# Kernel optimization log

Measured on AMD Instinct MI355X. Metric: run time of the kernel, lower is better.

## Reference

```python
import jax, jax.numpy as jnp
import numpy as np

N, E = 4096, 262144
IMG, EMB = 2048, 256        # img_feat_dim, embedding_dim*2
H, D = 4, 64                # heads, per-head out_channels (EMB//H for MHA too)
HID, C = 128, 2

def _sanitize(t):
    t = jnp.nan_to_num(t, nan=0.0, posinf=1000.0, neginf=-1000.0)
    return jnp.clip(t, -1000.0, 1000.0)

def _lrelu(t):
    return jax.nn.leaky_relu(t, 0.2)

def _instance_norm(y, eps=1e-5):
    # PyG InstanceNorm (affine=False), single graph: per-channel norm over nodes
    return (y - y.mean(0)) * jax.lax.rsqrt(y.var(0) + eps)

def _mha_causal(h, W_qkv, b_qkv, W_o, b_o):
    n = h.shape[0]
    qkv = h @ W_qkv.T + b_qkv
    q, k, v = jnp.split(qkv, 3, axis=-1)
    q = q.reshape(n, H, D); k = k.reshape(n, H, D); v = v.reshape(n, H, D)
    scores = jnp.einsum('qhd,khd->hqk', q, k) / np.float32(np.sqrt(D))
    mask = jnp.tril(jnp.ones((n, n), bool))
    scores = jnp.where(mask, scores, -jnp.inf)
    attn = jax.nn.softmax(scores, axis=-1)
    out = jnp.einsum('hqk,khd->qhd', attn, v).reshape(n, H * D)
    return out @ W_o.T + b_o

def _transformer_conv(xn, ei, Wq, bq, Wk, bk, Wv, bv, Ws, bs):
    # PyG TransformerConv: per-edge attention, softmax over incoming edges, +skip
    src, dst = ei[0], ei[1]
    n = xn.shape[0]
    q = (xn @ Wq.T + bq).reshape(n, H, D)
    k = (xn @ Wk.T + bk).reshape(n, H, D)
    v = (xn @ Wv.T + bv).reshape(n, H, D)
    logits = jnp.einsum('ehd,ehd->eh', q[dst], k[src]) / np.float32(np.sqrt(D))  # (E,H)
    amax = jax.ops.segment_max(logits, dst, num_segments=n)
    amax = jnp.where(jnp.isfinite(amax), amax, 0.0)
    ex = jnp.exp(logits - amax[dst])
    denom = jax.ops.segment_sum(ex, dst, num_segments=n)
    attn = ex / (denom[dst] + 1e-16)
    agg = jax.ops.segment_sum(attn[..., None] * v[src], dst, num_segments=n)
    return agg.reshape(n, H * D) + xn @ Ws.T + bs

def setup_inputs():
    key = jax.random.key(0)
    ks = jax.random.split(key, 20)
    w = lambda k, shape: jax.random.normal(k, shape, jnp.float32) * 0.02
    z = lambda d: jnp.zeros((d,), jnp.float32)
    return {
        'x': jax.random.normal(ks[0], (N, EMB), jnp.float32),
        'edge_index': jax.random.randint(ks[1], (2, E), 0, N),
        'img_feat': jax.random.normal(ks[2], (N, IMG), jnp.float32),
        'video_adj_list': jax.random.randint(ks[3], (2, E), 0, N),
        'W_img': w(ks[4], (EMB, IMG)), 'b_img': z(EMB),
        'W_qkv': w(ks[5], (3 * EMB, EMB)), 'b_qkv': z(3 * EMB),
        'W_o': w(ks[6], (EMB, EMB)), 'b_o': z(EMB),
        'Wq_o': w(ks[7], (H * D, EMB)), 'bq_o': z(H * D),
        'Wk_o': w(ks[8], (H * D, EMB)), 'bk_o': z(H * D),
        'Wv_o': w(ks[9], (H * D, EMB)), 'bv_o': z(H * D),
        'Ws_o': w(ks[10], (H * D, EMB)), 'bs_o': z(H * D),
        'Wq_a': w(ks[11], (H * D, EMB)), 'bq_a': z(H * D),
        'Wk_a': w(ks[12], (H * D, EMB)), 'bk_a': z(H * D),
        'Wv_a': w(ks[13], (H * D, EMB)), 'bv_a': z(H * D),
        'Ws_a': w(ks[14], (H * D, EMB)), 'bs_a': z(H * D),
        'W_c1': w(ks[15], (HID, 2 * H * D)), 'b_c1': z(HID),
        'W_c2': w(ks[16], (C, HID)), 'b_c2': z(C),
    }

def reference(x, edge_index, img_feat, video_adj_list, W_img, b_img, W_qkv, b_qkv, W_o, b_o,
              Wq_o, bq_o, Wk_o, bk_o, Wv_o, bv_o, Ws_o, bs_o,
              Wq_a, bq_a, Wk_a, bk_a, Wv_a, bv_a, Ws_a, bs_a,
              W_c1, b_c1, W_c2, b_c2):
    # x and edge_index are accepted but unused, matching the torch forward.
    h = img_feat @ W_img.T + b_img                                   # (N, EMB)
    h_attn = _sanitize(_mha_causal(h, W_qkv, b_qkv, W_o, b_o))
    fo = _sanitize(_lrelu(_instance_norm(
        _transformer_conv(h, video_adj_list, Wq_o, bq_o, Wk_o, bk_o, Wv_o, bv_o, Ws_o, bs_o))))
    fa = _sanitize(_lrelu(_instance_norm(
        _transformer_conv(h_attn, video_adj_list, Wq_a, bq_a, Wk_a, bk_a, Wv_a, bv_a, Ws_a, bs_a))))
    f = jnp.concatenate([fo, fa], axis=1)                            # (N, 512)
    f = _lrelu(f @ W_c1.T + b_c1)
    logits = f @ W_c2.T + b_c2
    probs = jax.nn.softmax(logits, axis=-1)
    return logits, probs
```

## Files before the change

### kernel.cpp

```cpp
#include <hip/hip_runtime.h>
#include <hip/hip_bf16.h>

typedef unsigned short u16;
typedef unsigned int   u32;
typedef __attribute__((ext_vector_type(8))) short short8;
typedef __attribute__((ext_vector_type(4))) float f32x4;

#define NN 4096
#define NE 262144
#define EMB 256
#define NH 4
#define HD 64

__device__ __forceinline__ float4 load4f(const float* p) { return *reinterpret_cast<const float4*>(p); }
__device__ __forceinline__ float sanitize_f(float v) {
  v = (v != v) ? 0.f : v;
  return fminf(fmaxf(v, -1000.f), 1000.f);
}
__device__ __forceinline__ u16 f2b_rne(float x) {
  u32 b = __float_as_uint(x);
  b += 0x7fff + ((b >> 16) & 1);
  return (u16)(b >> 16);
}
__device__ __forceinline__ u32 pack2(float a, float b) {
  return (u32)f2b_rne(a) | ((u32)f2b_rne(b) << 16);
}
__device__ __forceinline__ float b2f(u16 u) { return __uint_as_float((u32)u << 16); }

struct GTile {
  const float* W;
  const float* bias;
  float*       out;
  int          colOff;
  int          ldOut;
  int          obf16;
};
struct GArgs { GTile t[16]; };

template<int ACT>
__global__ __launch_bounds__(256) void gemm_mfma(const float* __restrict__ A, const GArgs ga, int K) {
  __shared__ short As[64 * 40];
  __shared__ short Bs[64 * 40];
  const int t = threadIdx.x;
  const int bm = blockIdx.x * 64;
  const GTile tl = ga.t[blockIdx.y];
  const int w = t >> 6, l = t & 63, g = l >> 4, r16 = l & 15;
  const int wr = w >> 1, wc = w & 1;
  const int lrow = t >> 2, lseg = (t & 3) * 8;

  const float* Ap = A + (size_t)(bm + lrow) * K + lseg;
  const float* Wp = tl.W + (size_t)lrow * K + lseg;

  f32x4 acc[2][2] = {{{0.f,0.f,0.f,0.f},{0.f,0.f,0.f,0.f}},{{0.f,0.f,0.f,0.f},{0.f,0.f,0.f,0.f}}};
  for (int k0 = 0; k0 < K; k0 += 32) {
    float4 a0 = load4f(Ap + k0), a1 = load4f(Ap + k0 + 4);
    float4 b0 = load4f(Wp + k0), b1 = load4f(Wp + k0 + 4);
    __syncthreads();
    *(uint4*)&As[lrow * 40 + lseg] =
        make_uint4(pack2(a0.x,a0.y), pack2(a0.z,a0.w), pack2(a1.x,a1.y), pack2(a1.z,a1.w));
    *(uint4*)&Bs[lrow * 40 + lseg] =
        make_uint4(pack2(b0.x,b0.y), pack2(b0.z,b0.w), pack2(b1.x,b1.y), pack2(b1.z,b1.w));
    __syncthreads();
    short8 af0 = *(const short8*)&As[(wr*32 +      r16) * 40 + 8*g];
    short8 af1 = *(const short8*)&As[(wr*32 + 16 + r16) * 40 + 8*g];
    short8 bf0 = *(const short8*)&Bs[(wc*32 +      r16) * 40 + 8*g];
    short8 bf1 = *(const short8*)&Bs[(wc*32 + 16 + r16) * 40 + 8*g];
    acc[0][0] = __builtin_amdgcn_mfma_f32_16x16x32_bf16(af0, bf0, acc[0][0], 0, 0, 0);
    acc[0][1] = __builtin_amdgcn_mfma_f32_16x16x32_bf16(af0, bf1, acc[0][1], 0, 0, 0);
    acc[1][0] = __builtin_amdgcn_mfma_f32_16x16x32_bf16(af1, bf0, acc[1][0], 0, 0, 0);
    acc[1][1] = __builtin_amdgcn_mfma_f32_16x16x32_bf16(af1, bf1, acc[1][1], 0, 0, 0);
  }
  const float bj[2] = { tl.bias[wc*32 + r16], tl.bias[wc*32 + 16 + r16] };
#pragma unroll
  for (int i = 0; i < 2; i++) {
#pragma unroll
    for (int j = 0; j < 2; j++) {
      int col  = tl.colOff + wc*32 + 16*j + r16;
      int row0 = bm + wr*32 + 16*i + 4*g;
      if (tl.obf16 == 2) {
        u16 pk[4];
#pragma unroll
        for (int r = 0; r < 4; r++) pk[r] = f2b_rne(acc[i][j][r] + bj[j]);
        *(uint2*)((u16*)tl.out + (size_t)col * tl.ldOut + row0) = *(uint2*)pk;
      } else {
#pragma unroll
        for (int r = 0; r < 4; r++) {
          float v = acc[i][j][r] + bj[j];
          if (ACT == 1) v = sanitize_f(v);
          if (ACT == 2) v = (v > 0.f) ? v : 0.2f * v;
          if (tl.obf16) ((u16*)tl.out)[(size_t)(row0 + r) * tl.ldOut + col] = f2b_rne(v);
          else          tl.out[(size_t)(row0 + r) * tl.ldOut + col] = v;
        }
      }
    }
  }
}

__global__ __launch_bounds__(256) void gemm_img_splitk(const float* __restrict__ A, const float* __restrict__ W,
                                                       float* __restrict__ part) {
  __shared__ short As[64 * 40];
  __shared__ short Bs[64 * 40];
  const int t = threadIdx.x;
  const int bm = blockIdx.x * 64, bn = blockIdx.y * 64, ks = blockIdx.z;
  const int w = t >> 6, l = t & 63, g = l >> 4, r16 = l & 15;
  const int wr = w >> 1, wc = w & 1;
  const int lrow = t >> 2, lseg = (t & 3) * 8;

  const float* Ap = A + (size_t)(bm + lrow) * 2048 + ks * 512 + lseg;
  const float* Wp = W + (size_t)(bn + lrow) * 2048 + ks * 512 + lseg;

  f32x4 acc[2][2] = {{{0.f,0.f,0.f,0.f},{0.f,0.f,0.f,0.f}},{{0.f,0.f,0.f,0.f},{0.f,0.f,0.f,0.f}}};
  for (int k0 = 0; k0 < 512; k0 += 32) {
    float4 a0 = load4f(Ap + k0), a1 = load4f(Ap + k0 + 4);
    float4 b0 = load4f(Wp + k0), b1 = load4f(Wp + k0 + 4);
    __syncthreads();
    *(uint4*)&As[lrow * 40 + lseg] =
        make_uint4(pack2(a0.x,a0.y), pack2(a0.z,a0.w), pack2(a1.x,a1.y), pack2(a1.z,a1.w));
    *(uint4*)&Bs[lrow * 40 + lseg] =
        make_uint4(pack2(b0.x,b0.y), pack2(b0.z,b0.w), pack2(b1.x,b1.y), pack2(b1.z,b1.w));
    __syncthreads();
    short8 af0 = *(const short8*)&As[(wr*32 +      r16) * 40 + 8*g];
    short8 af1 = *(const short8*)&As[(wr*32 + 16 + r16) * 40 + 8*g];
    short8 bf0 = *(const short8*)&Bs[(wc*32 +      r16) * 40 + 8*g];
    short8 bf1 = *(const short8*)&Bs[(wc*32 + 16 + r16) * 40 + 8*g];
    acc[0][0] = __builtin_amdgcn_mfma_f32_16x16x32_bf16(af0, bf0, acc[0][0], 0, 0, 0);
    acc[0][1] = __builtin_amdgcn_mfma_f32_16x16x32_bf16(af0, bf1, acc[0][1], 0, 0, 0);
    acc[1][0] = __builtin_amdgcn_mfma_f32_16x16x32_bf16(af1, bf0, acc[1][0], 0, 0, 0);
    acc[1][1] = __builtin_amdgcn_mfma_f32_16x16x32_bf16(af1, bf1, acc[1][1], 0, 0, 0);
  }
  float* op = part + (size_t)ks * (NN * 256);
#pragma unroll
  for (int i = 0; i < 2; i++) {
#pragma unroll
    for (int j = 0; j < 2; j++) {
      int col = bn + wc*32 + 16*j + r16;
#pragma unroll
      for (int r = 0; r < 4; r++) {
        int row = bm + wr*32 + 16*i + 4*g + r;
        op[(size_t)row * 256 + col] = acc[i][j][r];
      }
    }
  }
}
__global__ __launch_bounds__(256) void gemm_img_reduce(const float* __restrict__ part,
                                                       const float* __restrict__ bias,
                                                       float* __restrict__ h) {
  int idx = blockIdx.x * 256 + threadIdx.x;
  int row = idx >> 6, c4 = (idx & 63) * 4;
  size_t o = (size_t)row * 256 + c4;
  float4 s = load4f(part + o);
  float4 p1 = load4f(part + 1048576 + o);
  float4 p2 = load4f(part + 2097152 + o);
  float4 p3 = load4f(part + 3145728 + o);
  float4 bb = load4f(bias + c4);
  s.x += p1.x + p2.x + p3.x + bb.x;
  s.y += p1.y + p2.y + p3.y + bb.y;
  s.z += p1.z + p2.z + p3.z + bb.z;
  s.w += p1.w + p2.w + p3.w + bb.w;
  *(float4*)&h[o] = s;
}

#define KSTR 72
__global__ __launch_bounds__(256, 4) void mha_mfma3(const u16* __restrict__ qkb, const u16* __restrict__ vtb,
                                                    float* __restrict__ Opart, float* __restrict__ mspart) {
  __shared__ u16 Ks[64 * KSTR];
  __shared__ u16 Vs[64 * KSTR];
  const int bid = blockIdx.x;
  const int ks  = bid & 3;
  const int hh  = (bid >> 2) & 3;
  const int T   = 63 - (bid >> 4);
  const int q0  = T * 64;
  const int t   = threadIdx.x;
  const int w   = t >> 6, l = t & 63, g = l >> 4, r16 = l & 15;
  const int hofs = hh * 64;
  const int lrow = t >> 3, lc8 = (t & 7) * 8;

  const u16* qrow = qkb + (size_t)(q0 + 16 * w + r16) * 512 + hofs;
  short8 Qf0 = *(const short8*)&qrow[8 * g];
  short8 Qf1 = *(const short8*)&qrow[32 + 8 * g];

  f32x4 O0 = {0.f,0.f,0.f,0.f}, O1 = O0, O2 = O0, O3 = O0;
  float m = -INFINITY, ssum = 0.f;

  uint4 rk0, rk1, rv0, rv1;
  if (ks <= T) {
    int k0 = ks * 64;
    rk0 = *(const uint4*)&qkb[(size_t)(k0 + lrow) * 512 + 256 + hofs + lc8];
    rk1 = *(const uint4*)&qkb[(size_t)(k0 + 32 + lrow) * 512 + 256 + hofs + lc8];
    rv0 = *(const uint4*)&vtb[(size_t)(hofs + lrow) * 4096 + k0 + lc8];
    rv1 = *(const uint4*)&vtb[(size_t)(hofs + 32 + lrow) * 4096 + k0 + lc8];
  }
  for (int kt = ks; kt <= T; kt += 4) {
    __syncthreads();
    *(uint4*)&Ks[lrow * KSTR + lc8]        = rk0;
    *(uint4*)&Ks[(32 + lrow) * KSTR + lc8] = rk1;
    *(uint4*)&Vs[lrow * KSTR + lc8]        = rv0;
    *(uint4*)&Vs[(32 + lrow) * KSTR + lc8] = rv1;
    __syncthreads();
    if (kt + 4 <= T) {
      int k2 = (kt + 4) * 64;
      rk0 = *(const uint4*)&qkb[(size_t)(k2 + lrow) * 512 + 256 + hofs + lc8];
      rk1 = *(const uint4*)&qkb[(size_t)(k2 + 32 + lrow) * 512 + 256 + hofs + lc8];
      rv0 = *(const uint4*)&vtb[(size_t)(hofs + lrow) * 4096 + k2 + lc8];
      rv1 = *(const uint4*)&vtb[(size_t)(hofs + 32 + lrow) * 4096 + k2 + lc8];
    }
    f32x4 S0 = {0.f,0.f,0.f,0.f}, S1 = S0, S2 = S0, S3 = S0;
    {
      short8 a0 = *(const short8*)&Ks[(r16)      * KSTR + 8*g];
      short8 a1 = *(const short8*)&Ks[(16 + r16) * KSTR + 8*g];
      short8 a2 = *(const short8*)&Ks[(32 + r16) * KSTR + 8*g];
      short8 a3 = *(const short8*)&Ks[(48 + r16) * KSTR + 8*g];
      S0 = __builtin_amdgcn_mfma_f32_16x16x32_bf16(a0, Qf0, S0, 0, 0, 0);
      S1 = __builtin_amdgcn_mfma_f32_16x16x32_bf16(a1, Qf0, S1, 0, 0, 0);
      S2 = __builtin_amdgcn_mfma_f32_16x16x32_bf16(a2, Qf0, S2, 0, 0, 0);
      S3 = __builtin_amdgcn_mfma_f32_16x16x32_bf16(a3, Qf0, S3, 0, 0, 0);
      short8 b0 = *(const short8*)&Ks[(r16)      * KSTR + 32 + 8*g];
      short8 b1 = *(const short8*)&Ks[(16 + r16) * KSTR + 32 + 8*g];
      short8 b2 = *(const short8*)&Ks[(32 + r16) * KSTR + 32 + 8*g];
      short8 b3 = *(const short8*)&Ks[(48 + r16) * KSTR + 32 + 8*g];
      S0 = __builtin_amdgcn_mfma_f32_16x16x32_bf16(b0, Qf1, S0, 0, 0, 0);
      S1 = __builtin_amdgcn_mfma_f32_16x16x32_bf16(b1, Qf1, S1, 0, 0, 0);
      S2 = __builtin_amdgcn_mfma_f32_16x16x32_bf16(b2, Qf1, S2, 0, 0, 0);
      S3 = __builtin_amdgcn_mfma_f32_16x16x32_bf16(b3, Qf1, S3, 0, 0, 0);
    }
    float sc[4][4];
#pragma unroll
    for (int r = 0; r < 4; r++) {
      sc[0][r] = S0[r] * 0.125f; sc[1][r] = S1[r] * 0.125f;
      sc[2][r] = S2[r] * 0.125f; sc[3][r] = S3[r] * 0.125f;
    }
    if (kt == T) {
#pragma unroll
      for (int mb = 0; mb < 4; mb++)
#pragma unroll
        for (int r = 0; r < 4; r++)
          if (16 * mb + 4 * g + r > 16 * w + r16) sc[mb][r] = -INFINITY;
    }
    float tm = sc[0][0];
#pragma unroll
    for (int mb = 0; mb < 4; mb++)
#pragma unroll
      for (int r = 0; r < 4; r++) tm = fmaxf(tm, sc[mb][r]);
    tm = fmaxf(tm, __shfl_xor(tm, 16));
    tm = fmaxf(tm, __shfl_xor(tm, 32));
    float mn = fmaxf(m, tm);
    float ef = __expf(m - mn);
    float pv[4][4];
    float ps = 0.f;
#pragma unroll
    for (int mb = 0; mb < 4; mb++)
#pragma unroll
      for (int r = 0; r < 4; r++) { pv[mb][r] = __expf(sc[mb][r] - mn); ps += pv[mb][r]; }
    ps += __shfl_xor(ps, 16);
    ps += __shfl_xor(ps, 32);
    ssum = ssum * ef + ps;
    m = mn;
#pragma unroll
    for (int r = 0; r < 4; r++) {
      float efr = __shfl(ef, 4 * g + r);
      O0[r] *= efr; O1[r] *= efr; O2[r] *= efr; O3[r] *= efr;
    }
    u32 pk[2][4];
#pragma unroll
    for (int c = 0; c < 2; c++)
#pragma unroll
      for (int rs = 0; rs < 4; rs++) pk[c][rs] = pack2(pv[2 * c][rs], pv[2 * c + 1][rs]);
    short8 ap[2];
#pragma unroll
    for (int c = 0; c < 2; c++) {
#pragma unroll
      for (int jb = 0; jb < 2; jb++) {
        int x = 2 * g + jb;
        int hi = x >> 2;
        int src = r16 + 16 * (x & 3);
#pragma unroll
        for (int rs = 0; rs < 4; rs++) {
          u32 v = __shfl(pk[c][rs], src);
          ap[c][jb * 4 + rs] = (short)(hi ? (v >> 16) : (v & 0xffff));
        }
      }
    }
    {
      short8 V00 = *(const short8*)&Vs[(r16)      * KSTR + 8*g];
      short8 V10 = *(const short8*)&Vs[(16 + r16) * KSTR + 8*g];
      short8 V20 = *(const short8*)&Vs[(32 + r16) * KSTR + 8*g];
      short8 V30 = *(const short8*)&Vs[(48 + r16) * KSTR + 8*g];
      O0 = __builtin_amdgcn_mfma_f32_16x16x32_bf16(ap[0], V00, O0, 0, 0, 0);
      O1 = __builtin_amdgcn_mfma_f32_16x16x32_bf16(ap[0], V10, O1, 0, 0, 0);
      O2 = __builtin_amdgcn_mfma_f32_16x16x32_bf16(ap[0], V20, O2, 0, 0, 0);
      O3 = __builtin_amdgcn_mfma_f32_16x16x32_bf16(ap[0], V30, O3, 0, 0, 0);
      short8 V01 = *(const short8*)&Vs[(r16)      * KSTR + 32 + 8*g];
      short8 V11 = *(const short8*)&Vs[(16 + r16) * KSTR + 32 + 8*g];
      short8 V21 = *(const short8*)&Vs[(32 + r16) * KSTR + 32 + 8*g];
      short8 V31 = *(const short8*)&Vs[(48 + r16) * KSTR + 32 + 8*g];
      O0 = __builtin_amdgcn_mfma_f32_16x16x32_bf16(ap[1], V01, O0, 0, 0, 0);
      O1 = __builtin_amdgcn_mfma_f32_16x16x32_bf16(ap[1], V11, O1, 0, 0, 0);
      O2 = __builtin_amdgcn_mfma_f32_16x16x32_bf16(ap[1], V21, O2, 0, 0, 0);
      O3 = __builtin_amdgcn_mfma_f32_16x16x32_bf16(ap[1], V31, O3, 0, 0, 0);
    }
  }

  size_t ob = (size_t)bid * 4096;
#pragma unroll
  for (int r = 0; r < 4; r++) {
    int q = 16 * w + 4 * g + r;
    Opart[ob + q * 64 + r16]      = O0[r];
    Opart[ob + q * 64 + 16 + r16] = O1[r];
    Opart[ob + q * 64 + 32 + r16] = O2[r];
    Opart[ob + q * 64 + 48 + r16] = O3[r];
  }
  if (l < 16) {
    mspart[bid * 128 + 16 * w + l]      = m;
    mspart[bid * 128 + 64 + 16 * w + l] = ssum;
  }
}

__global__ __launch_bounds__(256) void mha_merge3(const float* __restrict__ Opart, const float* __restrict__ mspart,
                                                  float* __restrict__ out) {
  int mb = blockIdx.x;
  int h = mb & 3, T = mb >> 2;
  int bid0 = ((63 - T) << 4) | (h << 2);
  int t = threadIdx.x;
  int q = t >> 2, dbase = (t & 3) * 16;
  float mm[4], ss[4];
#pragma unroll
  for (int i = 0; i < 4; i++) {
    mm[i] = mspart[(bid0 + i) * 128 + q];
    ss[i] = mspart[(bid0 + i) * 128 + 64 + q];
  }
  float M = fmaxf(fmaxf(mm[0], mm[1]), fmaxf(mm[2], mm[3]));
  float e[4];
  float S = 0.f;
#pragma unroll
  for (int i = 0; i < 4; i++) {
    e[i] = (mm[i] == -INFINITY) ? 0.f : __expf(mm[i] - M);
    S += e[i] * ss[i];
  }
  float inv = 1.f / S;
  float* Y = out + (size_t)(T * 64 + q) * EMB + h * 64 + dbase;
#pragma unroll
  for (int i = 0; i < 4; i++) {
    float4 a0 = load4f(Opart + (size_t)(bid0 + 0) * 4096 + q * 64 + dbase + 4 * i);
    float4 a1 = load4f(Opart + (size_t)(bid0 + 1) * 4096 + q * 64 + dbase + 4 * i);
    float4 a2 = load4f(Opart + (size_t)(bid0 + 2) * 4096 + q * 64 + dbase + 4 * i);
    float4 a3 = load4f(Opart + (size_t)(bid0 + 3) * 4096 + q * 64 + dbase + 4 * i);
    float4 r;
    r.x = (e[0]*a0.x + e[1]*a1.x + e[2]*a2.x + e[3]*a3.x) * inv;
    r.y = (e[0]*a0.y + e[1]*a1.y + e[2]*a2.y + e[3]*a3.y) * inv;
    r.z = (e[0]*a0.z + e[1]*a1.z + e[2]*a2.z + e[3]*a3.z) * inv;
    r.w = (e[0]*a0.w + e[1]*a1.w + e[2]*a2.w + e[3]*a3.w) * inv;
    *(float4*)(Y + 4 * i) = r;
  }
}

__global__ void zero_i32(int* p, int n) {
  int i = blockIdx.x * 256 + threadIdx.x;
  if (i < n) p[i] = 0;
}
__global__ void hist_dst(const int* __restrict__ adj, int* __restrict__ cnt) {
  int e = blockIdx.x * 256 + threadIdx.x;
  if (e < NE) atomicAdd(&cnt[adj[NE + e]], 1);
}
__global__ __launch_bounds__(1024) void scan4096(const int* __restrict__ cnt, int* __restrict__ indptr,
                                                 int* __restrict__ cursor) {
  int t = threadIdx.x;
  int4 c = *reinterpret_cast<const int4*>(cnt + t * 4);
  int s0 = c.x, s1 = s0 + c.y, s2 = s1 + c.z, s3 = s2 + c.w;
  int lane = t & 63, w = t >> 6;
  int x = s3;
#pragma unroll
  for (int off = 1; off < 64; off <<= 1) {
    int y = __shfl_up(x, off);
    if (lane >= off) x += y;
  }
  __shared__ int wsum[16];
  if (lane == 63) wsum[w] = x;
  __syncthreads();
  if (t == 0) {
    int acc = 0;
    for (int i = 0; i < 16; i++) { int tv = wsum[i]; wsum[i] = acc; acc += tv; }
  }
  __syncthreads();
  int b = wsum[w] + x - s3;
  indptr[t*4+0] = b;      indptr[t*4+1] = b + s0;
  indptr[t*4+2] = b + s1; indptr[t*4+3] = b + s2;
  cursor[t*4+0] = b;      cursor[t*4+1] = b + s0;
  cursor[t*4+2] = b + s1; cursor[t*4+3] = b + s2;
  if (t == 1023) indptr[4096] = b + s3;
}
__global__ void scatter_edges(const int* __restrict__ adj, int* __restrict__ cursor, int* __restrict__ esrc) {
  int e = blockIdx.x * 256 + threadIdx.x;
  if (e < NE) {
    int dst = adj[NE + e];
    int pos = atomicAdd(&cursor[dst], 1);
    esrc[pos] = adj[e];
  }
}

__global__ __launch_bounds__(256, 4) void conv_agg(const float* __restrict__ qb, const u16* __restrict__ kb,
                                                   const u16* __restrict__ vb, const int* __restrict__ indptr,
                                                   const int* __restrict__ esrc, float* __restrict__ y) {
  __shared__ float q_s[EMB];
  __shared__ float sc_s[NH][64];
  __shared__ float p_s[NH][64];
  __shared__ int   s_s[64];
  int n = blockIdx.x;
  int tid = threadIdx.x;
  int h = tid >> 6, lane = tid & 63;
  int lr8 = lane >> 3;
  int lseg = (lane & 7) * 8;
  q_s[tid] = qb[(size_t)n * EMB + tid] * 0.125f;
  int start = indptr[n], end = indptr[n + 1];
  __syncthreads();
  const float* qh = &q_s[h * HD];
  float q8[8];
#pragma unroll
  for (int j = 0; j < 8; j++) q8[j] = qh[lseg + j];
  float m = -INFINITY, s = 0.f;
  float o0 = 0.f, o1 = 0.f, o2 = 0.f, o3 = 0.f;
  for (int p0 = start; p0 < end; p0 += 64) {
    int nk = end - p0; if (nk > 64) nk = 64;
    if (h == 0) s_s[lane] = (lane < nk) ? esrc[p0 + lane] : 0;
    __syncthreads();
#pragma unroll
    for (int pass = 0; pass < 8; pass++) {
      int row = pass * 8 + lr8;
      int src = s_s[row];
      short8 k8 = *(const short8*)&kb[(size_t)src * EMB + h * HD + lseg];
      float a0 = fmaf(b2f((u16)k8[0]), q8[0], 0.f);
      float a1 = fmaf(b2f((u16)k8[1]), q8[1], 0.f);
      a0 = fmaf(b2f((u16)k8[2]), q8[2], a0);
      a1 = fmaf(b2f((u16)k8[3]), q8[3], a1);
      a0 = fmaf(b2f((u16)k8[4]), q8[4], a0);
      a1 = fmaf(b2f((u16)k8[5]), q8[5], a1);
      a0 = fmaf(b2f((u16)k8[6]), q8[6], a0);
      a1 = fmaf(b2f((u16)k8[7]), q8[7], a1);
      float acc = a0 + a1;
      acc += __shfl_xor(acc, 1);
      acc += __shfl_xor(acc, 2);
      acc += __shfl_xor(acc, 4);
      if ((lane & 7) == 0) sc_s[h][row] = (row < nk) ? acc : -INFINITY;
    }
    float sc = sc_s[h][lane];
    float bm = sc;
#pragma unroll
    for (int off = 32; off; off >>= 1) bm = fmaxf(bm, __shfl_xor(bm, off));
    float mn = fmaxf(m, bm);
    float ef = __expf(m - mn);
    float p = __expf(sc - mn);
    float ps = p;
#pragma unroll
    for (int off = 32; off; off >>= 1) ps += __shfl_xor(ps, off);
    s = s * ef + ps;
    m = mn;
    o0 *= ef; o1 *= ef; o2 *= ef; o3 *= ef;
    p_s[h][lane] = p;
    const u16* vcol = vb + h * HD + lane;
    int nk4 = (nk + 3) & ~3;
    for (int jj = 0; jj < nk4; jj += 4) {
      float pa = p_s[h][jj],   pb = p_s[h][jj+1];
      float pc = p_s[h][jj+2], pd = p_s[h][jj+3];
      int sa = s_s[jj], sb = s_s[jj+1], scx = s_s[jj+2], sd = s_s[jj+3];
      o0 = fmaf(pa, b2f(vcol[(size_t)sa  * EMB]), o0);
      o1 = fmaf(pb, b2f(vcol[(size_t)sb  * EMB]), o1);
      o2 = fmaf(pc, b2f(vcol[(size_t)scx * EMB]), o2);
      o3 = fmaf(pd, b2f(vcol[(size_t)sd  * EMB]), o3);
    }
    __syncthreads();
  }
  float o = (o0 + o1) + (o2 + o3);
  float agg = o / (s + 1e-16f);
  y[(size_t)n * EMB + h * HD + lane] += agg;
}

__global__ __launch_bounds__(256) void colstats_partial(const float* __restrict__ y, float* __restrict__ part) {
  int c = threadIdx.x;
  int r0 = blockIdx.x * 128;
  float s = 0.f, q = 0.f;
  for (int r = r0; r < r0 + 128; r++) {
    float v = y[(size_t)r * EMB + c];
    s += v; q = fmaf(v, v, q);
  }
  part[blockIdx.x * 512 + c] = s;
  part[blockIdx.x * 512 + 256 + c] = q;
}
__global__ __launch_bounds__(256) void colstats_final(const float* __restrict__ part, float* __restrict__ stats) {
  int c = threadIdx.x;
  float s = 0.f, q = 0.f;
  for (int b = 0; b < 32; b++) { s += part[b * 512 + c]; q += part[b * 512 + 256 + c]; }
  float mean = s * (1.f / 4096.f);
  float var  = q * (1.f / 4096.f) - mean * mean;
  stats[c] = mean;
  stats[256 + c] = rsqrtf(var + 1e-5f);
}
__global__ __launch_bounds__(256) void norm_apply(const float* __restrict__ y, const float* __restrict__ stats,
                                                  float* __restrict__ f, int colOff) {
  int c = threadIdx.x;
  float mean = stats[c], rstd = stats[256 + c];
  int r0 = blockIdx.x * 16;
  for (int r = r0; r < r0 + 16; r++) {
    float v = (y[(size_t)r * EMB + c] - mean) * rstd;
    v = (v > 0.f) ? v : 0.2f * v;
    v = sanitize_f(v);
    f[(size_t)r * 512 + colOff + c] = v;
  }
}

__global__ __launch_bounds__(256) void final_softmax(const float* __restrict__ f1, const float* __restrict__ W2,
                                                     const float* __restrict__ b2, float* __restrict__ out) {
  int w = threadIdx.x >> 6, lane = threadIdx.x & 63;
  int row = blockIdx.x * 4 + w;
  const float* fr = f1 + (size_t)row * 128;
  float x0 = fr[lane], x1 = fr[lane + 64];
  float p0 = x0 * W2[lane]       + x1 * W2[64 + lane];
  float p1 = x0 * W2[128 + lane] + x1 * W2[192 + lane];
#pragma unroll
  for (int off = 32; off; off >>= 1) { p0 += __shfl_xor(p0, off); p1 += __shfl_xor(p1, off); }
  if (lane == 0) {
    float l0 = p0 + b2[0], l1 = p1 + b2[1];
    float mx = fmaxf(l0, l1);
    float e0 = __expf(l0 - mx), e1 = __expf(l1 - mx);
    float inv = 1.f / (e0 + e1);
    out[(size_t)row * 2 + 0] = l0;
    out[(size_t)row * 2 + 1] = l1;
    out[8192 + (size_t)row * 2 + 0] = e0 * inv;
    out[8192 + (size_t)row * 2 + 1] = e1 * inv;
  }
}

extern "C" void kernel_launch(void* const* d_in, const int* in_sizes, int n_in,
                              void* d_out, int out_size, void* d_ws, size_t ws_size,
                              hipStream_t stream) {
  const float* img   = (const float*)d_in[2];
  const int*   adj   = (const int*)d_in[3];
  const float* W_img = (const float*)d_in[4];  const float* b_img = (const float*)d_in[5];
  const float* W_qkv = (const float*)d_in[6];  const float* b_qkv = (const float*)d_in[7];
  const float* W_o   = (const float*)d_in[8];  const float* b_o   = (const float*)d_in[9];
  const float* Wq_o  = (const float*)d_in[10]; const float* bq_o  = (const float*)d_in[11];
  const float* Wk_o  = (const float*)d_in[12]; const float* bk_o  = (const float*)d_in[13];
  const float* Wv_o  = (const float*)d_in[14]; const float* bv_o  = (const float*)d_in[15];
  const float* Ws_o  = (const float*)d_in[16]; const float* bs_o  = (const float*)d_in[17];
  const float* Wq_a  = (const float*)d_in[18]; const float* bq_a  = (const float*)d_in[19];
  const float* Wk_a  = (const float*)d_in[20]; const float* bk_a  = (const float*)d_in[21];
  const float* Wv_a  = (const float*)d_in[22]; const float* bv_a  = (const float*)d_in[23];
  const float* Ws_a  = (const float*)d_in[24]; const float* bs_a  = (const float*)d_in[25];
  const float* W_c1  = (const float*)d_in[26]; const float* b_c1  = (const float*)d_in[27];
  const float* W_c2  = (const float*)d_in[28]; const float* b_c2  = (const float*)d_in[29];

  char* ws = (char*)d_ws;
  float* h     = (float*)(ws + 0);
  float* hattn = (float*)(ws + (4ull << 20));
  float* qkv   = (float*)(ws + (8ull << 20));
  float* y     = (float*)(ws + (20ull << 20));
  float* f     = (float*)(ws + (24ull << 20));
  float* f1    = (float*)(ws + (32ull << 20));
  int*   indptr= (int*)  (ws + (34ull << 20));
  int*   cursor= (int*)  (ws + (34ull << 20) + 20480);
  int*   esrc  = (int*)  (ws + (34ull << 20) + 40960);
  float* part  = (float*)(ws + (34ull << 20) + 40960 + (1ull << 20));
  float* stats = (float*)(ws + (34ull << 20) + 40960 + (1ull << 20) + 65536);

  u16* qkb = (u16*)hattn;
  u16* vtb = (u16*)f1;

  float* imgpart = qkv;
  float* Opart   = qkv;
  float* mspart  = (float*)esrc;
  float* ymha    = f;

  float* qb   = qkv;
  u16*   kb16 = (u16*)(ws + (12ull << 20));
  u16*   vb16 = (u16*)(ws + (14ull << 20));

  dim3 b256(256);

  gemm_img_splitk<<<dim3(64, 4, 4), b256, 0, stream>>>(img, W_img, imgpart);
  gemm_img_reduce<<<1024, b256, 0, stream>>>(imgpart, b_img, h);
  {
    GArgs ga;
    for (int i = 0; i < 8; i++)
      ga.t[i]  = { W_qkv + (size_t)i * 64 * 256, b_qkv + i * 64, (float*)qkb, i * 64, 512, 1 };
    for (int i = 8; i < 12; i++)
      ga.t[i]  = { W_qkv + (size_t)i * 64 * 256, b_qkv + i * 64, (float*)vtb, (i - 8) * 64, 4096, 2 };
    gemm_mfma<0><<<dim3(64, 12), b256, 0, stream>>>(h, ga, 256);
  }
  mha_mfma3<<<1024, b256, 0, stream>>>(qkb, vtb, Opart, mspart);
  mha_merge3<<<256, b256, 0, stream>>>(Opart, mspart, ymha);
  {
    GArgs ga;
    for (int i = 0; i < 4; i++)
      ga.t[i] = { W_o + (size_t)i * 64 * 256, b_o + i * 64, hattn, i * 64, 256, 0 };
    gemm_mfma<1><<<dim3(64, 4), b256, 0, stream>>>(ymha, ga, 256);
  }
  zero_i32<<<16, b256, 0, stream>>>(cursor, NN);
  hist_dst<<<NE / 256, b256, 0, stream>>>(adj, cursor);
  scan4096<<<1, 1024, 0, stream>>>(cursor, indptr, cursor);
  scatter_edges<<<NE / 256, b256, 0, stream>>>(adj, cursor, esrc);

  {
    const float* Wg[4] = { Wq_o, Wk_o, Wv_o, Ws_o };
    const float* bg[4] = { bq_o, bk_o, bv_o, bs_o };
    float*       og[4] = { qb, (float*)kb16, (float*)vb16, y };
    const int    bf[4] = { 0, 1, 1, 0 };
    GArgs ga;
    for (int i = 0; i < 16; i++) {
      int gdx = i >> 2, li = i & 3;
      ga.t[i] = { Wg[gdx] + (size_t)li * 64 * 256, bg[gdx] + li * 64, og[gdx], li * 64, 256, bf[gdx] };
    }
    gemm_mfma<0><<<dim3(64, 16), b256, 0, stream>>>(h, ga, 256);
  }
  conv_agg<<<NN, b256, 0, stream>>>(qb, kb16, vb16, indptr, esrc, y);
  colstats_partial<<<32, b256, 0, stream>>>(y, part);
  colstats_final<<<1, b256, 0, stream>>>(part, stats);
  norm_apply<<<256, b256, 0, stream>>>(y, stats, f, 0);

  {
    const float* Wg[4] = { Wq_a, Wk_a, Wv_a, Ws_a };
    const float* bg[4] = { bq_a, bk_a, bv_a, bs_a };
    float*       og[4] = { qb, (float*)kb16, (float*)vb16, y };
    const int    bf[4] = { 0, 1, 1, 0 };
    GArgs ga;
    for (int i = 0; i < 16; i++) {
      int gdx = i >> 2, li = i & 3;
      ga.t[i] = { Wg[gdx] + (size_t)li * 64 * 256, bg[gdx] + li * 64, og[gdx], li * 64, 256, bf[gdx] };
    }
    gemm_mfma<0><<<dim3(64, 16), b256, 0, stream>>>(hattn, ga, 256);
  }
  conv_agg<<<NN, b256, 0, stream>>>(qb, kb16, vb16, indptr, esrc, y);
  colstats_partial<<<32, b256, 0, stream>>>(y, part);
  colstats_final<<<1, b256, 0, stream>>>(part, stats);
  norm_apply<<<256, b256, 0, stream>>>(y, stats, f, 256);

  {
    GArgs ga;
    for (int i = 0; i < 2; i++)
      ga.t[i] = { W_c1 + (size_t)i * 64 * 512, b_c1 + i * 64, f1, i * 64, 128, 0 };
    gemm_mfma<2><<<dim3(64, 2), b256, 0, stream>>>(f, ga, 512);
  }
  final_softmax<<<NN / 4, b256, 0, stream>>>(f1, W_c2, b_c2, (float*)d_out);
}
```

Baseline: 273.5 us.

## Batch both TransformerConv branches into shared GEMM, aggregation and norm launches

The two TransformerConv branches (original and attention-refined features) now run together. Their Q/K/V/skip projections go through one 32-tile GEMM launch, made possible by giving each tile its own A pointer. Aggregation, column stats and normalization each become one launch covering both paths, and the colstats_final kernel is folded into norm_apply. V is now stored in fp32 rather than bf16, which removes the bf16 rounding on V but doubles the bytes of the gathered V reads, and the workspace layout is expanded so each branch has separate buffers.

```diff
diff --git a/kernel.cpp b/kernel.cpp
--- a/kernel.cpp
+++ b/kernel.cpp
@@ -28,6 +28,7 @@
 __device__ __forceinline__ float b2f(u16 u) { return __uint_as_float((u32)u << 16); }
 
 struct GTile {
+  const float* A;
   const float* W;
   const float* bias;
   float*       out;
@@ -35,10 +36,10 @@
   int          ldOut;
   int          obf16;
 };
-struct GArgs { GTile t[16]; };
+struct GArgs { GTile t[32]; };
 
 template<int ACT>
-__global__ __launch_bounds__(256) void gemm_mfma(const float* __restrict__ A, const GArgs ga, int K) {
+__global__ __launch_bounds__(256) void gemm_mfma(const GArgs ga, int K) {
   __shared__ short As[64 * 40];
   __shared__ short Bs[64 * 40];
   const int t = threadIdx.x;
@@ -48,7 +49,7 @@
   const int wr = w >> 1, wc = w & 1;
   const int lrow = t >> 2, lseg = (t & 3) * 8;
 
-  const float* Ap = A + (size_t)(bm + lrow) * K + lseg;
+  const float* Ap = tl.A + (size_t)(bm + lrow) * K + lseg;
   const float* Wp = tl.W + (size_t)lrow * K + lseg;
 
   f32x4 acc[2][2] = {{{0.f,0.f,0.f,0.f},{0.f,0.f,0.f,0.f}},{{0.f,0.f,0.f,0.f},{0.f,0.f,0.f,0.f}}};
@@ -397,14 +398,22 @@
   }
 }
 
-__global__ __launch_bounds__(256, 4) void conv_agg(const float* __restrict__ qb, const u16* __restrict__ kb,
-                                                   const u16* __restrict__ vb, const int* __restrict__ indptr,
-                                                   const int* __restrict__ esrc, float* __restrict__ y) {
+__global__ __launch_bounds__(256, 4) void conv_agg2(const float* __restrict__ qbO, const float* __restrict__ qbA,
+                                                    const u16* __restrict__ kbO, const u16* __restrict__ kbA,
+                                                    const float* __restrict__ vbO, const float* __restrict__ vbA,
+                                                    const int* __restrict__ indptr, const int* __restrict__ esrc,
+                                                    float* __restrict__ yO, float* __restrict__ yA) {
   __shared__ float q_s[EMB];
   __shared__ float sc_s[NH][64];
   __shared__ float p_s[NH][64];
   __shared__ int   s_s[64];
-  int n = blockIdx.x;
+  int bid = blockIdx.x;
+  int path = bid >> 12;
+  int n = bid & 4095;
+  const float* qb = path ? qbA : qbO;
+  const u16*   kb = path ? kbA : kbO;
+  const float* vb = path ? vbA : vbO;
+  float*       y  = path ? yA  : yO;
   int tid = threadIdx.x;
   int h = tid >> 6, lane = tid & 63;
   int lr8 = lane >> 3;
@@ -455,16 +464,16 @@
     m = mn;
     o0 *= ef; o1 *= ef; o2 *= ef; o3 *= ef;
     p_s[h][lane] = p;
-    const u16* vcol = vb + h * HD + lane;
+    const float* vcol = vb + h * HD + lane;
     int nk4 = (nk + 3) & ~3;
     for (int jj = 0; jj < nk4; jj += 4) {
       float pa = p_s[h][jj],   pb = p_s[h][jj+1];
       float pc = p_s[h][jj+2], pd = p_s[h][jj+3];
       int sa = s_s[jj], sb = s_s[jj+1], scx = s_s[jj+2], sd = s_s[jj+3];
-      o0 = fmaf(pa, b2f(vcol[(size_t)sa  * EMB]), o0);
-      o1 = fmaf(pb, b2f(vcol[(size_t)sb  * EMB]), o1);
-      o2 = fmaf(pc, b2f(vcol[(size_t)scx * EMB]), o2);
-      o3 = fmaf(pd, b2f(vcol[(size_t)sd  * EMB]), o3);
+      o0 = fmaf(pa, vcol[(size_t)sa  * EMB], o0);
+      o1 = fmaf(pb, vcol[(size_t)sb  * EMB], o1);
+      o2 = fmaf(pc, vcol[(size_t)scx * EMB], o2);
+      o3 = fmaf(pd, vcol[(size_t)sd  * EMB], o3);
     }
     __syncthreads();
   }
@@ -473,31 +482,35 @@
   y[(size_t)n * EMB + h * HD + lane] += agg;
 }
 
-__global__ __launch_bounds__(256) void colstats_partial(const float* __restrict__ y, float* __restrict__ part) {
+__global__ __launch_bounds__(256) void colstats_partial2(const float* __restrict__ yO, const float* __restrict__ yA,
+                                                         float* __restrict__ part) {
+  int bid = blockIdx.x;
+  int path = bid >> 5, pb = bid & 31;
+  const float* y = path ? yA : yO;
   int c = threadIdx.x;
-  int r0 = blockIdx.x * 128;
+  int r0 = pb * 128;
   float s = 0.f, q = 0.f;
   for (int r = r0; r < r0 + 128; r++) {
     float v = y[(size_t)r * EMB + c];
     s += v; q = fmaf(v, v, q);
   }
-  part[blockIdx.x * 512 + c] = s;
-  part[blockIdx.x * 512 + 256 + c] = q;
-}
-__global__ __launch_bounds__(256) void colstats_final(const float* __restrict__ part, float* __restrict__ stats) {
+  part[(size_t)path * 16384 + pb * 512 + c] = s;
+  part[(size_t)path * 16384 + pb * 512 + 256 + c] = q;
+}
+__global__ __launch_bounds__(256) void norm_apply2(const float* __restrict__ yO, const float* __restrict__ yA,
+                                                   const float* __restrict__ part, float* __restrict__ f) {
+  int bid = blockIdx.x;
+  int path = bid >> 8, rb = bid & 255;
+  const float* y = path ? yA : yO;
+  const float* pp = part + (size_t)path * 16384;
   int c = threadIdx.x;
   float s = 0.f, q = 0.f;
-  for (int b = 0; b < 32; b++) { s += part[b * 512 + c]; q += part[b * 512 + 256 + c]; }
+  for (int b = 0; b < 32; b++) { s += pp[b * 512 + c]; q += pp[b * 512 + 256 + c]; }
   float mean = s * (1.f / 4096.f);
   float var  = q * (1.f / 4096.f) - mean * mean;
-  stats[c] = mean;
-  stats[256 + c] = rsqrtf(var + 1e-5f);
-}
-__global__ __launch_bounds__(256) void norm_apply(const float* __restrict__ y, const float* __restrict__ stats,
-                                                  float* __restrict__ f, int colOff) {
-  int c = threadIdx.x;
-  float mean = stats[c], rstd = stats[256 + c];
-  int r0 = blockIdx.x * 16;
+  float rstd = rsqrtf(var + 1e-5f);
+  int r0 = rb * 16;
+  int colOff = path * 256;
   for (int r = r0; r < r0 + 16; r++) {
     float v = (y[(size_t)r * EMB + c] - mean) * rstd;
     v = (v > 0.f) ? v : 0.2f * v;
@@ -549,28 +562,28 @@
 
   char* ws = (char*)d_ws;
   float* h     = (float*)(ws + 0);
-  float* hattn = (float*)(ws + (4ull << 20));
-  float* qkv   = (float*)(ws + (8ull << 20));
-  float* y     = (float*)(ws + (20ull << 20));
-  float* f     = (float*)(ws + (24ull << 20));
-  float* f1    = (float*)(ws + (32ull << 20));
-  int*   indptr= (int*)  (ws + (34ull << 20));
-  int*   cursor= (int*)  (ws + (34ull << 20) + 20480);
-  int*   esrc  = (int*)  (ws + (34ull << 20) + 40960);
-  float* part  = (float*)(ws + (34ull << 20) + 40960 + (1ull << 20));
-  float* stats = (float*)(ws + (34ull << 20) + 40960 + (1ull << 20) + 65536);
-
-  u16* qkb = (u16*)hattn;
-  u16* vtb = (u16*)f1;
-
-  float* imgpart = qkv;
-  float* Opart   = qkv;
+  float* hattn = (float*)(ws + (4ull  << 20));
+  float* qbO   = (float*)(ws + (8ull  << 20));
+  u16*   kbO   = (u16*)  (ws + (12ull << 20));
+  float* vbO   = (float*)(ws + (14ull << 20));
+  float* qbA   = (float*)(ws + (18ull << 20));
+  u16*   kbA   = (u16*)  (ws + (22ull << 20));
+  float* vbA   = (float*)(ws + (24ull << 20));
+  float* yO    = (float*)(ws + (28ull << 20));
+  float* yA    = (float*)(ws + (32ull << 20));
+  float* f     = (float*)(ws + (36ull << 20));
+  float* f1    = (float*)(ws + (44ull << 20));
+  int*   indptr= (int*)  (ws + (46ull << 20));
+  int*   cursor= (int*)  (ws + (46ull << 20) + 20480);
+  int*   esrc  = (int*)  (ws + (46ull << 20) + 40960);
+  float* part  = (float*)(ws + (46ull << 20) + 40960 + (1ull << 20));
+
+  u16*   qkb     = (u16*)hattn;
+  u16*   vtb     = (u16*)f1;
+  float* imgpart = qbO;
+  float* Opart   = qbO;
   float* mspart  = (float*)esrc;
-  float* ymha    = f;
-
-  float* qb   = qkv;
-  u16*   kb16 = (u16*)(ws + (12ull << 20));
-  u16*   vb16 = (u16*)(ws + (14ull << 20));
+  float* ymha    = yO;
 
   dim3 b256(256);
 
@@ -579,18 +592,18 @@
   {
     GArgs ga;
     for (int i = 0; i < 8; i++)
-      ga.t[i]  = { W_qkv + (size_t)i * 64 * 256, b_qkv + i * 64, (float*)qkb, i * 64, 512, 1 };
+      ga.t[i]  = { h, W_qkv + (size_t)i * 64 * 256, b_qkv + i * 64, (float*)qkb, i * 64, 512, 1 };
     for (int i = 8; i < 12; i++)
-      ga.t[i]  = { W_qkv + (size_t)i * 64 * 256, b_qkv + i * 64, (float*)vtb, (i - 8) * 64, 4096, 2 };
-    gemm_mfma<0><<<dim3(64, 12), b256, 0, stream>>>(h, ga, 256);
+      ga.t[i]  = { h, W_qkv + (size_t)i * 64 * 256, b_qkv + i * 64, (float*)vtb, (i - 8) * 64, 4096, 2 };
+    gemm_mfma<0><<<dim3(64, 12), b256, 0, stream>>>(ga, 256);
   }
   mha_mfma3<<<1024, b256, 0, stream>>>(qkb, vtb, Opart, mspart);
   mha_merge3<<<256, b256, 0, stream>>>(Opart, mspart, ymha);
   {
     GArgs ga;
     for (int i = 0; i < 4; i++)
-      ga.t[i] = { W_o + (size_t)i * 64 * 256, b_o + i * 64, hattn, i * 64, 256, 0 };
-    gemm_mfma<1><<<dim3(64, 4), b256, 0, stream>>>(ymha, ga, 256);
+      ga.t[i] = { ymha, W_o + (size_t)i * 64 * 256, b_o + i * 64, hattn, i * 64, 256, 0 };
+    gemm_mfma<1><<<dim3(64, 4), b256, 0, stream>>>(ga, 256);
   }
   zero_i32<<<16, b256, 0, stream>>>(cursor, NN);
   hist_dst<<<NE / 256, b256, 0, stream>>>(adj, cursor);
@@ -598,44 +611,26 @@
   scatter_edges<<<NE / 256, b256, 0, stream>>>(adj, cursor, esrc);
 
   {
-    const float* Wg[4] = { Wq_o, Wk_o, Wv_o, Ws_o };
-    const float* bg[4] = { bq_o, bk_o, bv_o, bs_o };
-    float*       og[4] = { qb, (float*)kb16, (float*)vb16, y };
-    const int    bf[4] = { 0, 1, 1, 0 };
+    const float* Wg[8] = { Wq_o, Wk_o, Wv_o, Ws_o, Wq_a, Wk_a, Wv_a, Ws_a };
+    const float* bg[8] = { bq_o, bk_o, bv_o, bs_o, bq_a, bk_a, bv_a, bs_a };
+    float*       og[8] = { qbO, (float*)kbO, vbO, yO, qbA, (float*)kbA, vbA, yA };
+    const float* Ag[8] = { h, h, h, h, hattn, hattn, hattn, hattn };
+    const int    bf[8] = { 0, 1, 0, 0, 0, 1, 0, 0 };
     GArgs ga;
-    for (int i = 0; i < 16; i++) {
+    for (int i = 0; i < 32; i++) {
       int gdx = i >> 2, li = i & 3;
-      ga.t[i] = { Wg[gdx] + (size_t)li * 64 * 256, bg[gdx] + li * 64, og[gdx], li * 64, 256, bf[gdx] };
-    }
-    gemm_mfma<0><<<dim3(64, 16), b256, 0, stream>>>(h, ga, 256);
-  }
-  conv_agg<<<NN, b256, 0, stream>>>(qb, kb16, vb16, indptr, esrc, y);
-  colstats_partial<<<32, b256, 0, stream>>>(y, part);
-  colstats_final<<<1, b256, 0, stream>>>(part, stats);
-  norm_apply<<<256, b256, 0, stream>>>(y, stats, f, 0);
-
-  {
-    const float* Wg[4] = { Wq_a, Wk_a, Wv_a, Ws_a };
-    const float* bg[4] = { bq_a, bk_a, bv_a, bs_a };
-    float*       og[4] = { qb, (float*)kb16, (float*)vb16, y };
-    const int    bf[4] = { 0, 1, 1, 0 };
-    GArgs ga;
-    for (int i = 0; i < 16; i++) {
-      int gdx = i >> 2, li = i & 3;
-      ga.t[i] = { Wg[gdx] + (size_t)li * 64 * 256, bg[gdx] + li * 64, og[gdx], li * 64, 256, bf[gdx] };
-    }
-    gemm_mfma<0><<<dim3(64, 16), b256, 0, stream>>>(hattn, ga, 256);
-  }
-  conv_agg<<<NN, b256, 0, stream>>>(qb, kb16, vb16, indptr, esrc, y);
-  colstats_partial<<<32, b256, 0, stream>>>(y, part);
-  colstats_final<<<1, b256, 0, stream>>>(part, stats);
-  norm_apply<<<256, b256, 0, stream>>>(y, stats, f, 256);
-
+      ga.t[i] = { Ag[gdx], Wg[gdx] + (size_t)li * 64 * 256, bg[gdx] + li * 64, og[gdx], li * 64, 256, bf[gdx] };
+    }
+    gemm_mfma<0><<<dim3(64, 32), b256, 0, stream>>>(ga, 256);
+  }
+  conv_agg2<<<8192, b256, 0, stream>>>(qbO, qbA, kbO, kbA, vbO, vbA, indptr, esrc, yO, yA);
+  colstats_partial2<<<64, b256, 0, stream>>>(yO, yA, part);
+  norm_apply2<<<512, b256, 0, stream>>>(yO, yA, part, f);
   {
     GArgs ga;
     for (int i = 0; i < 2; i++)
-      ga.t[i] = { W_c1 + (size_t)i * 64 * 512, b_c1 + i * 64, f1, i * 64, 128, 0 };
-    gemm_mfma<2><<<dim3(64, 2), b256, 0, stream>>>(f, ga, 512);
+      ga.t[i] = { f, W_c1 + (size_t)i * 64 * 512, b_c1 + i * 64, f1, i * 64, 128, 0 };
+    gemm_mfma<2><<<dim3(64, 2), b256, 0, stream>>>(ga, 512);
   }
   final_softmax<<<NN / 4, b256, 0, stream>>>(f1, W_c2, b_c2, (float*)d_out);
 }
```

After: 250.8 us. 8.3% less time.
